# Kernel tuning notes

Measured on AMD Instinct MI355X. Metric: run time of the kernel, lower is better.

The kernel has to match this reference:

```python
import jax, jax.numpy as jnp
import numpy as np

LOC_SCOPE = 3.0
LOC_BIN_SIZE = 0.5
NUM_HEAD_BIN = 12
PER_LOC_BIN = int(LOC_SCOPE / LOC_BIN_SIZE) * 2  # 12
REG_C = PER_LOC_BIN * 4 + 1 + NUM_HEAD_BIN * 2 + 3  # 76


def decode_bbox_target(roi, reg, anchor):
    # roi: (M, 3) point centers; reg: (M, 76); anchor: (3,)
    b = PER_LOC_BIN
    f32 = reg.dtype
    x_bin = jnp.argmax(reg[:, 0:b], axis=1)
    z_bin = jnp.argmax(reg[:, b:2 * b], axis=1)
    pos_x = x_bin.astype(f32) * LOC_BIN_SIZE + LOC_BIN_SIZE / 2 - LOC_SCOPE
    pos_z = z_bin.astype(f32) * LOC_BIN_SIZE + LOC_BIN_SIZE / 2 - LOC_SCOPE
    # fine xz residual: gather residual of the argmax bin (batch_dims=1 gather)
    x_res = jnp.take_along_axis(reg[:, 2 * b:3 * b], x_bin[:, None], axis=1)[:, 0] * LOC_BIN_SIZE
    z_res = jnp.take_along_axis(reg[:, 3 * b:4 * b], z_bin[:, None], axis=1)[:, 0] * LOC_BIN_SIZE
    pos_x = pos_x + x_res
    pos_z = pos_z + z_res
    start = 4 * b
    # y by direct offset (get_y_by_bin=False)
    pos_y = roi[:, 1] + reg[:, start]
    start = start + 1
    # heading: coarse bin argmax + fine residual gather (get_ry_fine=False)
    ry_bin = jnp.argmax(reg[:, start:start + NUM_HEAD_BIN], axis=1)
    ry_res_norm = jnp.take_along_axis(
        reg[:, start + NUM_HEAD_BIN:start + 2 * NUM_HEAD_BIN], ry_bin[:, None], axis=1)[:, 0]
    angle_per_class = 2.0 * np.pi / NUM_HEAD_BIN
    ry = (ry_bin.astype(f32) * angle_per_class + ry_res_norm * (angle_per_class / 2)) % (2.0 * np.pi)
    ry = jnp.where(ry > np.pi, ry - 2.0 * np.pi, ry)
    # size: residual around anchor
    hwl = reg[:, start + 2 * NUM_HEAD_BIN:start + 2 * NUM_HEAD_BIN + 3] * anchor + anchor
    # roi has 3 cols -> no rotate_pc_along_y branch; shift x,z by roi center
    box = jnp.concatenate([
        (pos_x + roi[:, 0])[:, None],
        pos_y[:, None],
        (pos_z + roi[:, 2])[:, None],
        hwl,
        ry[:, None],
    ], axis=1)  # (M, 7)
    return box


def setup_inputs() -> dict:
    key = jax.random.key(0)
    k1, k2, k3 = jax.random.split(key, 3)
    B, N = 8, 131072
    rpn_scores = jax.random.normal(k1, (B, N), dtype=jnp.float32)
    rpn_reg = jax.random.normal(k2, (B, N, REG_C), dtype=jnp.float32)
    xyz = jax.random.normal(k3, (B, N, 3), dtype=jnp.float32) * 20.0
    anchor_size = jnp.array([1.52563191462, 1.62856739989, 3.88311640418], dtype=jnp.float32)
    return {"rpn_scores": rpn_scores, "rpn_reg": rpn_reg, "xyz": xyz, "anchor_size": anchor_size}


def reference(rpn_scores, rpn_reg, xyz, anchor_size):
    B, N, C = rpn_reg.shape
    props = decode_bbox_target(xyz.reshape(-1, 3), rpn_reg.reshape(-1, C), anchor_size)
    props = props.reshape(B, N, 7)
    # post_process: lift y to box top-center (y + h/2)
    props = jnp.concatenate([props[..., :1], props[..., 1:2] + props[..., 3:4] / 2, props[..., 2:]], axis=-1)
    # score-descending ordering of proposals (per batch row)
    order = jnp.argsort(-rpn_scores, axis=1)  # (B, N)
    boxes = jnp.take_along_axis(props, order[..., None], axis=1)
    scores = jnp.take_along_axis(rpn_scores, order, axis=1)
    # pack boxes+scores: (B, N, 8)
    return jnp.concatenate([boxes, scores[..., None]], axis=-1)
```

## Files before the change

kernel.cpp:

```cpp
#include <hip/hip_runtime.h>
#include <math.h>

#define N_PER   131072
#define NBATCH  8
#define REGC    76
#define TOTAL   (NBATCH * N_PER)
#define TILE    2048
#define NBLKSEG (N_PER / TILE)
#define BINS    256
#define SCTH    512
#define CHUNKS  (TILE / SCTH)

__device__ __forceinline__ unsigned desc_key(float f) {
    unsigned u = __float_as_uint(f);
    return (u & 0x80000000u) ? u : ~(u | 0x80000000u);
}

__global__ __launch_bounds__(256) void decode_kernel(
    const float* __restrict__ scores, const float* __restrict__ reg,
    const float* __restrict__ xyz, const float* __restrict__ anchor,
    float* __restrict__ boxes8)
{
    int p = blockIdx.x * 256 + threadIdx.x;
    const float* r = reg + (size_t)p * REGC;
    const float4* r4 = (const float4*)r;

    float4 q0 = r4[0],  q1 = r4[1],  q2 = r4[2];
    float4 q3 = r4[3],  q4 = r4[4],  q5 = r4[5];
    float4 s0 = r4[12], s1 = r4[13], s2 = r4[14], s3 = r4[15];
    float4 tt = r4[18];

    float xa[12] = {q0.x,q0.y,q0.z,q0.w, q1.x,q1.y,q1.z,q1.w, q2.x,q2.y,q2.z,q2.w};
    float za[12] = {q3.x,q3.y,q3.z,q3.w, q4.x,q4.y,q4.z,q4.w, q5.x,q5.y,q5.z,q5.w};
    float ra[12] = {s0.y,s0.z,s0.w, s1.x,s1.y,s1.z,s1.w, s2.x,s2.y,s2.z,s2.w, s3.x};

    int xb = 0; float xm = xa[0];
#pragma unroll
    for (int c = 1; c < 12; ++c) { if (xa[c] > xm) { xm = xa[c]; xb = c; } }
    int zb = 0; float zm = za[0];
#pragma unroll
    for (int c = 1; c < 12; ++c) { if (za[c] > zm) { zm = za[c]; zb = c; } }
    int yb = 0; float ym = ra[0];
#pragma unroll
    for (int c = 1; c < 12; ++c) { if (ra[c] > ym) { ym = ra[c]; yb = c; } }

    float x_res  = r[24 + xb];
    float z_res  = r[36 + zb];
    float ry_res = r[61 + yb];

    float rx = xyz[(size_t)p * 3 + 0];
    float ryy = xyz[(size_t)p * 3 + 1];
    float rz = xyz[(size_t)p * 3 + 2];
    float a0 = anchor[0], a1 = anchor[1], a2 = anchor[2];

    const float APC    = (float)(2.0 * M_PI / 12.0);
    const float HAPC   = (float)(M_PI / 12.0);
    const float TWO_PI = (float)(2.0 * M_PI);
    const float PI_F   = (float)M_PI;

    float vry = __fadd_rn(__fmul_rn((float)yb, APC), __fmul_rn(ry_res, HAPC));
    float m = fmodf(vry, TWO_PI);
    if (m < 0.0f) m += TWO_PI;
    if (m > PI_F) m -= TWO_PI;

    float h = tt.y * a0 + a0;
    float w = tt.z * a1 + a1;
    float l = tt.w * a2 + a2;

    float ox = (((float)xb * 0.5f + 0.25f - 3.0f) + x_res * 0.5f) + rx;
    float oz = (((float)zb * 0.5f + 0.25f - 3.0f) + z_res * 0.5f) + rz;
    float oy = (ryy + s0.x) + h * 0.5f;

    float sc = scores[p];

    float4* ob = (float4*)(boxes8 + (size_t)p * 8);
    ob[0] = make_float4(ox, oy, oz, h);
    ob[1] = make_float4(w, l, m, sc);
}

template<int PASS>
__global__ __launch_bounds__(256) void hist_kernel(
    const float* __restrict__ scores, const unsigned* __restrict__ keyIn,
    unsigned short* __restrict__ hist)
{
    __shared__ unsigned h[BINS];
    int tid = threadIdx.x;
    h[tid] = 0;
    __syncthreads();
    int id = blockIdx.x;
    int seg = id & 7, blk = id >> 3;
    size_t base = (size_t)seg * N_PER + (size_t)blk * TILE;
#pragma unroll
    for (int c = 0; c < TILE / 256; ++c) {
        unsigned key;
        if (PASS == 0) key = desc_key(scores[base + c * 256 + tid]);
        else           key = keyIn[base + c * 256 + tid];
        atomicAdd(&h[(key >> (PASS * 8)) & 255u], 1u);
    }
    __syncthreads();
    hist[(size_t)(seg * NBLKSEG + blk) * BINS + tid] = (unsigned short)h[tid];
}

template<int PASS>
__global__ __launch_bounds__(512) void scatter_kernel(
    const float* __restrict__ scores,
    const unsigned* __restrict__ keyIn, const unsigned* __restrict__ payIn,
    unsigned* __restrict__ keyOut, unsigned* __restrict__ payOut,
    const unsigned short* __restrict__ hist)
{
    __shared__ unsigned whist[CHUNKS * 8][BINS];
    __shared__ unsigned skey[TILE];
    __shared__ unsigned spay[TILE];
    __shared__ unsigned offs[BINS];
    __shared__ unsigned lexcl[BINS];
    __shared__ unsigned wsum[4];

    const int tid  = threadIdx.x;
    const int wave = tid >> 6, lane = tid & 63;
    const unsigned long long lmask = (1ull << lane) - 1ull;
    const int id  = blockIdx.x;
    const int seg = id & 7, blk = id >> 3;
    const size_t segbase = (size_t)seg * N_PER;
    const int gbase = blk * TILE;

    unsigned my_pref = 0, my_tot = 0;
    if (tid < BINS) {
        const unsigned short* hp = hist + (size_t)(seg * NBLKSEG) * BINS + tid;
        unsigned pref = 0, tot = 0;
#pragma unroll
        for (int b = 0; b < NBLKSEG; ++b) {
            unsigned c = hp[(size_t)b * BINS];
            tot += c;
            if (b < blk) pref += c;
        }
        my_pref = pref; my_tot = tot;
    } else {
        int z = tid - BINS;
        unsigned* wf = &whist[0][0];
#pragma unroll
        for (int k = 0; k < CHUNKS * 8; ++k) wf[k * BINS + z] = 0;
    }
    __syncthreads();

    unsigned my_base = 0;
    if (tid < BINS) {
        unsigned v = my_tot;
#pragma unroll
        for (int o = 1; o < 64; o <<= 1) {
            unsigned n = __shfl_up(v, o, 64);
            if (lane >= o) v += n;
        }
        if (lane == 63) wsum[wave] = v;
        my_base = v - my_tot;
    }
    __syncthreads();
    if (tid < BINS) {
        unsigned add = 0;
#pragma unroll
        for (int w2 = 0; w2 < 4; ++w2) { if (w2 < wave) add += wsum[w2]; }
        offs[tid] = my_base + add + my_pref;
    }

    unsigned kr[CHUNKS], pr[CHUNKS], dr[CHUNKS], rr[CHUNKS];
#pragma unroll
    for (int c = 0; c < CHUNKS; ++c) {
        int idx = c * SCTH + tid;
        unsigned key, pay;
        if (PASS == 0) {
            key = desc_key(scores[segbase + gbase + idx]);
            pay = (unsigned)(gbase + idx);
        } else {
            key = keyIn[segbase + gbase + idx];
            pay = payIn[segbase + gbase + idx];
        }
        unsigned d = (key >> (PASS * 8)) & 255u;
        unsigned long long peers = ~0ull;
#pragma unroll
        for (int b = 0; b < 8; ++b) {
            unsigned long long vote = __ballot((d >> b) & 1u);
            peers &= ((d >> b) & 1u) ? vote : ~vote;
        }
        unsigned rank = (unsigned)__popcll(peers & lmask);
        if (rank == 0) whist[c * 8 + wave][d] = (unsigned)__popcll(peers);
        kr[c] = key; pr[c] = pay; dr[c] = d; rr[c] = rank;
    }
    __syncthreads();

    unsigned my_ltot = 0, my_lpart = 0;
    if (tid < BINS) {
        unsigned run = 0;
#pragma unroll
        for (int i = 0; i < CHUNKS * 8; ++i) {
            unsigned v = whist[i][tid];
            whist[i][tid] = run;
            run += v;
        }
        my_ltot = run;
        unsigned v = run;
#pragma unroll
        for (int o = 1; o < 64; o <<= 1) {
            unsigned n = __shfl_up(v, o, 64);
            if (lane >= o) v += n;
        }
        if (lane == 63) wsum[wave] = v;
        my_lpart = v - my_ltot;
    }
    __syncthreads();
    if (tid < BINS) {
        unsigned add = 0;
#pragma unroll
        for (int w2 = 0; w2 < 4; ++w2) { if (w2 < wave) add += wsum[w2]; }
        lexcl[tid] = my_lpart + add;
    }
    __syncthreads();

#pragma unroll
    for (int c = 0; c < CHUNKS; ++c) {
        unsigned j = lexcl[dr[c]] + whist[c * 8 + wave][dr[c]] + rr[c];
        skey[j] = kr[c];
        spay[j] = pr[c];
    }
    __syncthreads();

#pragma unroll
    for (int c = 0; c < CHUNKS; ++c) {
        unsigned j = (unsigned)(c * SCTH + tid);
        unsigned key = skey[j];
        unsigned pay = spay[j];
        unsigned d = (key >> (PASS * 8)) & 255u;
        unsigned g = offs[d] + (j - lexcl[d]);
        if (PASS < 3) keyOut[segbase + g] = key;
        payOut[segbase + g] = pay;
    }
}

__global__ __launch_bounds__(256) void gather_kernel(
    const float* __restrict__ boxes8, const unsigned* __restrict__ pay,
    float* __restrict__ out)
{
    int id = blockIdx.x;
    int seg = id & 7;
    int bi  = id >> 3;
    int t   = threadIdx.x;
    int rowInSeg = bi * 128 + (t >> 1);
    int half = t & 1;
    size_t row = (size_t)seg * N_PER + rowInSeg;
    unsigned i = pay[row];
    const float4* src = (const float4*)(boxes8 + ((size_t)seg * N_PER + i) * 8);
    float4 v = src[half];
    ((float4*)(out + row * 8))[half] = v;
}

extern "C" void kernel_launch(void* const* d_in, const int* in_sizes, int n_in,
                              void* d_out, int out_size, void* d_ws, size_t ws_size,
                              hipStream_t stream)
{
    const float* scores = (const float*)d_in[0];
    const float* reg    = (const float*)d_in[1];
    const float* xyz    = (const float*)d_in[2];
    const float* anchor = (const float*)d_in[3];
    float* out = (float*)d_out;

    char* ws = (char*)d_ws;
    float*    boxes8 = (float*)ws;
    size_t    off    = (size_t)TOTAL * 8 * sizeof(float);
    unsigned* keyA = (unsigned*)(ws + off); off += (size_t)TOTAL * 4;
    unsigned* payA = (unsigned*)(ws + off); off += (size_t)TOTAL * 4;
    unsigned* keyB = (unsigned*)(ws + off); off += (size_t)TOTAL * 4;
    unsigned* payB = (unsigned*)(ws + off); off += (size_t)TOTAL * 4;
    unsigned short* hist = (unsigned short*)(ws + off);
    off += (size_t)NBATCH * NBLKSEG * BINS * sizeof(unsigned short);
    (void)ws_size; (void)in_sizes; (void)n_in; (void)out_size;

    decode_kernel<<<TOTAL / 256, 256, 0, stream>>>(scores, reg, xyz, anchor, boxes8);

    const int NG = NBATCH * NBLKSEG;

    hist_kernel<0><<<NG, 256, 0, stream>>>(scores, nullptr, hist);
    scatter_kernel<0><<<NG, SCTH, 0, stream>>>(scores, nullptr, nullptr,
                                               keyB, payB, hist);
    hist_kernel<1><<<NG, 256, 0, stream>>>(nullptr, keyB, hist);
    scatter_kernel<1><<<NG, SCTH, 0, stream>>>(nullptr, keyB, payB,
                                               keyA, payA, hist);
    hist_kernel<2><<<NG, 256, 0, stream>>>(nullptr, keyA, hist);
    scatter_kernel<2><<<NG, SCTH, 0, stream>>>(nullptr, keyA, payA,
                                               keyB, payB, hist);
    hist_kernel<3><<<NG, 256, 0, stream>>>(nullptr, keyB, hist);
    scatter_kernel<3><<<NG, SCTH, 0, stream>>>(nullptr, keyB, payB,
                                               nullptr, payA, hist);

    gather_kernel<<<NBATCH * (N_PER / 128), 256, 0, stream>>>(boxes8, payA, out);
}
```

Measured before the change: 523.3 us.

## Fuse radix histograms into one pass, add decoupled lookback, spread decode across passes

Computes all four digit histograms in a single kernel, replacing the four per-pass histogram launches. A decoupled-lookback chain across blocks computes each block's per-bin prefix within a scatter pass. The decode work is split into quarters: one quarter runs in the histogram kernel and the rest in scatter passes 0-2. The final gather is folded into the last scatter pass. Keys are also narrowed to 16 and 8 bits in later passes to cut traffic. The aim is fewer launches and less memory traffic, at the cost of spin-wait lookback that relies on blocks being scheduled in a forward-progress order.

```diff
diff --git a/kernel.cpp b/kernel.cpp
--- a/kernel.cpp
+++ b/kernel.cpp
@@ -10,18 +10,28 @@
 #define BINS    256
 #define SCTH    512
 #define CHUNKS  (TILE / SCTH)
+#define NG      (NBATCH * NBLKSEG)
+#define QROWS   (TOTAL / 4)
 
 __device__ __forceinline__ unsigned desc_key(float f) {
     unsigned u = __float_as_uint(f);
     return (u & 0x80000000u) ? u : ~(u | 0x80000000u);
 }
 
-__global__ __launch_bounds__(256) void decode_kernel(
-    const float* __restrict__ scores, const float* __restrict__ reg,
-    const float* __restrict__ xyz, const float* __restrict__ anchor,
+__device__ __forceinline__ unsigned wave_incl_scan(unsigned v, int lane) {
+#pragma unroll
+    for (int o = 1; o < 64; o <<= 1) {
+        unsigned n = __shfl_up(v, o, 64);
+        if (lane >= o) v += n;
+    }
+    return v;
+}
+
+__device__ __forceinline__ void decode_one(
+    int p, const float* __restrict__ scores, const float* __restrict__ reg,
+    const float* __restrict__ xyz, float a0, float a1, float a2,
     float* __restrict__ boxes8)
 {
-    int p = blockIdx.x * 256 + threadIdx.x;
     const float* r = reg + (size_t)p * REGC;
     const float4* r4 = (const float4*)r;
 
@@ -48,10 +58,9 @@
     float z_res  = r[36 + zb];
     float ry_res = r[61 + yb];
 
-    float rx = xyz[(size_t)p * 3 + 0];
+    float rx  = xyz[(size_t)p * 3 + 0];
     float ryy = xyz[(size_t)p * 3 + 1];
-    float rz = xyz[(size_t)p * 3 + 2];
-    float a0 = anchor[0], a1 = anchor[1], a2 = anchor[2];
+    float rz  = xyz[(size_t)p * 3 + 2];
 
     const float APC    = (float)(2.0 * M_PI / 12.0);
     const float HAPC   = (float)(M_PI / 12.0);
@@ -78,39 +87,51 @@
     ob[1] = make_float4(w, l, m, sc);
 }
 
-template<int PASS>
-__global__ __launch_bounds__(256) void hist_kernel(
-    const float* __restrict__ scores, const unsigned* __restrict__ keyIn,
-    unsigned short* __restrict__ hist)
+__global__ __launch_bounds__(256) void hist_decode_kernel(
+    const float* __restrict__ scores, const float* __restrict__ reg,
+    const float* __restrict__ xyz, const float* __restrict__ anchor,
+    float* __restrict__ boxes8, unsigned* __restrict__ ghist)
 {
-    __shared__ unsigned h[BINS];
+    __shared__ unsigned lh[4][BINS];
     int tid = threadIdx.x;
-    h[tid] = 0;
+    lh[0][tid] = 0; lh[1][tid] = 0; lh[2][tid] = 0; lh[3][tid] = 0;
     __syncthreads();
     int id = blockIdx.x;
     int seg = id & 7, blk = id >> 3;
     size_t base = (size_t)seg * N_PER + (size_t)blk * TILE;
 #pragma unroll
     for (int c = 0; c < TILE / 256; ++c) {
-        unsigned key;
-        if (PASS == 0) key = desc_key(scores[base + c * 256 + tid]);
-        else           key = keyIn[base + c * 256 + tid];
-        atomicAdd(&h[(key >> (PASS * 8)) & 255u], 1u);
-    }
-    __syncthreads();
-    hist[(size_t)(seg * NBLKSEG + blk) * BINS + tid] = (unsigned short)h[tid];
+        unsigned k = desc_key(scores[base + c * 256 + tid]);
+        atomicAdd(&lh[0][k & 255u], 1u);
+        atomicAdd(&lh[1][(k >> 8) & 255u], 1u);
+        atomicAdd(&lh[2][(k >> 16) & 255u], 1u);
+        atomicAdd(&lh[3][k >> 24], 1u);
+    }
+    __syncthreads();
+#pragma unroll
+    for (int p = 0; p < 4; ++p)
+        atomicAdd(&ghist[(size_t)(seg * 4 + p) * BINS + tid], lh[p][tid]);
+
+    float a0 = anchor[0], a1 = anchor[1], a2 = anchor[2];
+    int r0 = id * 512 + tid;
+    decode_one(r0,       scores, reg, xyz, a0, a1, a2, boxes8);
+    decode_one(r0 + 256, scores, reg, xyz, a0, a1, a2, boxes8);
 }
 
 template<int PASS>
-__global__ __launch_bounds__(512) void scatter_kernel(
+__global__ __launch_bounds__(SCTH) void scatter_kernel(
     const float* __restrict__ scores,
-    const unsigned* __restrict__ keyIn, const unsigned* __restrict__ payIn,
-    unsigned* __restrict__ keyOut, unsigned* __restrict__ payOut,
-    const unsigned short* __restrict__ hist)
+    const void* __restrict__ keyIn, const unsigned* __restrict__ payIn,
+    void* __restrict__ keyOut, unsigned* __restrict__ payOut,
+    const unsigned* __restrict__ ghist, unsigned* __restrict__ status,
+    const float* __restrict__ reg, const float* __restrict__ xyz,
+    const float* __restrict__ anchor, float* __restrict__ boxes8,
+    float* __restrict__ out)
 {
     __shared__ unsigned whist[CHUNKS * 8][BINS];
-    __shared__ unsigned skey[TILE];
+    __shared__ unsigned skey[(PASS < 3) ? TILE : 1];
     __shared__ unsigned spay[TILE];
+    __shared__ unsigned char sdig[TILE];
     __shared__ unsigned offs[BINS];
     __shared__ unsigned lexcl[BINS];
     __shared__ unsigned wsum[4];
@@ -123,17 +144,12 @@
     const size_t segbase = (size_t)seg * N_PER;
     const int gbase = blk * TILE;
 
-    unsigned my_pref = 0, my_tot = 0;
+    unsigned my_part = 0;
     if (tid < BINS) {
-        const unsigned short* hp = hist + (size_t)(seg * NBLKSEG) * BINS + tid;
-        unsigned pref = 0, tot = 0;
-#pragma unroll
-        for (int b = 0; b < NBLKSEG; ++b) {
-            unsigned c = hp[(size_t)b * BINS];
-            tot += c;
-            if (b < blk) pref += c;
-        }
-        my_pref = pref; my_tot = tot;
+        unsigned tot = ghist[(size_t)(seg * 4 + PASS) * BINS + tid];
+        unsigned v = wave_incl_scan(tot, lane);
+        if (lane == 63) wsum[wave] = v;
+        my_part = v - tot;
     } else {
         int z = tid - BINS;
         unsigned* wf = &whist[0][0];
@@ -141,39 +157,34 @@
         for (int k = 0; k < CHUNKS * 8; ++k) wf[k * BINS + z] = 0;
     }
     __syncthreads();
-
-    unsigned my_base = 0;
-    if (tid < BINS) {
-        unsigned v = my_tot;
-#pragma unroll
-        for (int o = 1; o < 64; o <<= 1) {
-            unsigned n = __shfl_up(v, o, 64);
-            if (lane >= o) v += n;
-        }
-        if (lane == 63) wsum[wave] = v;
-        my_base = v - my_tot;
-    }
-    __syncthreads();
     if (tid < BINS) {
         unsigned add = 0;
 #pragma unroll
         for (int w2 = 0; w2 < 4; ++w2) { if (w2 < wave) add += wsum[w2]; }
-        offs[tid] = my_base + add + my_pref;
+        offs[tid] = my_part + add;
     }
 
     unsigned kr[CHUNKS], pr[CHUNKS], dr[CHUNKS], rr[CHUNKS];
 #pragma unroll
     for (int c = 0; c < CHUNKS; ++c) {
         int idx = c * SCTH + tid;
-        unsigned key, pay;
+        unsigned outkey = 0, d, pay;
         if (PASS == 0) {
-            key = desc_key(scores[segbase + gbase + idx]);
+            unsigned k = desc_key(scores[segbase + gbase + idx]);
+            outkey = k; d = k & 255u;
             pay = (unsigned)(gbase + idx);
+        } else if (PASS == 1) {
+            unsigned k = ((const unsigned*)keyIn)[segbase + gbase + idx];
+            outkey = k >> 16; d = (k >> 8) & 255u;
+            pay = payIn[segbase + gbase + idx];
+        } else if (PASS == 2) {
+            unsigned k = ((const unsigned short*)keyIn)[segbase + gbase + idx];
+            outkey = k >> 8; d = k & 255u;
+            pay = payIn[segbase + gbase + idx];
         } else {
-            key = keyIn[segbase + gbase + idx];
+            d = ((const unsigned char*)keyIn)[segbase + gbase + idx];
             pay = payIn[segbase + gbase + idx];
         }
-        unsigned d = (key >> (PASS * 8)) & 255u;
         unsigned long long peers = ~0ull;
 #pragma unroll
         for (int b = 0; b < 8; ++b) {
@@ -182,11 +193,11 @@
         }
         unsigned rank = (unsigned)__popcll(peers & lmask);
         if (rank == 0) whist[c * 8 + wave][d] = (unsigned)__popcll(peers);
-        kr[c] = key; pr[c] = pay; dr[c] = d; rr[c] = rank;
-    }
-    __syncthreads();
-
-    unsigned my_ltot = 0, my_lpart = 0;
+        kr[c] = outkey; pr[c] = pay; dr[c] = d; rr[c] = rank;
+    }
+    __syncthreads();
+
+    unsigned my_lrun = 0, my_lpart = 0;
     if (tid < BINS) {
         unsigned run = 0;
 #pragma unroll
@@ -195,15 +206,36 @@
             whist[i][tid] = run;
             run += v;
         }
-        my_ltot = run;
-        unsigned v = run;
-#pragma unroll
-        for (int o = 1; o < 64; o <<= 1) {
-            unsigned n = __shfl_up(v, o, 64);
-            if (lane >= o) v += n;
-        }
-        if (lane == 63) wsum[wave] = v;
-        my_lpart = v - my_ltot;
+        my_lrun = run;
+        unsigned* stp = status + (size_t)(seg * NBLKSEG) * BINS + tid;
+        unsigned pref = 0;
+        if (blk == 0) {
+            __hip_atomic_store(&stp[(size_t)blk * BINS],
+                (2u << 20) | ((unsigned)PASS << 18) | run,
+                __ATOMIC_RELEASE, __HIP_MEMORY_SCOPE_AGENT);
+        } else {
+            __hip_atomic_store(&stp[(size_t)blk * BINS],
+                (1u << 20) | ((unsigned)PASS << 18) | run,
+                __ATOMIC_RELEASE, __HIP_MEMORY_SCOPE_AGENT);
+            int b = blk - 1;
+            for (;;) {
+                unsigned v;
+                do {
+                    v = __hip_atomic_load(&stp[(size_t)b * BINS],
+                        __ATOMIC_ACQUIRE, __HIP_MEMORY_SCOPE_AGENT);
+                } while (((v >> 18) & 3u) != (unsigned)PASS || (v >> 20) == 0u);
+                pref += v & 0x3FFFFu;
+                if ((v >> 20) == 2u) break;
+                --b;
+            }
+            __hip_atomic_store(&stp[(size_t)blk * BINS],
+                (2u << 20) | ((unsigned)PASS << 18) | (pref + run),
+                __ATOMIC_RELEASE, __HIP_MEMORY_SCOPE_AGENT);
+        }
+        offs[tid] += pref;
+        unsigned v2 = wave_incl_scan(run, lane);
+        if (lane == 63) wsum[wave] = v2;
+        my_lpart = v2 - run;
     }
     __syncthreads();
     if (tid < BINS) {
@@ -217,38 +249,40 @@
 #pragma unroll
     for (int c = 0; c < CHUNKS; ++c) {
         unsigned j = lexcl[dr[c]] + whist[c * 8 + wave][dr[c]] + rr[c];
-        skey[j] = kr[c];
+        if (PASS < 3) skey[j] = kr[c];
         spay[j] = pr[c];
+        sdig[j] = (unsigned char)dr[c];
     }
     __syncthreads();
 
 #pragma unroll
     for (int c = 0; c < CHUNKS; ++c) {
         unsigned j = (unsigned)(c * SCTH + tid);
-        unsigned key = skey[j];
+        unsigned d = sdig[j];
+        unsigned g = offs[d] + (j - lexcl[d]);
         unsigned pay = spay[j];
-        unsigned d = (key >> (PASS * 8)) & 255u;
-        unsigned g = offs[d] + (j - lexcl[d]);
-        if (PASS < 3) keyOut[segbase + g] = key;
-        payOut[segbase + g] = pay;
-    }
-}
-
-__global__ __launch_bounds__(256) void gather_kernel(
-    const float* __restrict__ boxes8, const unsigned* __restrict__ pay,
-    float* __restrict__ out)
-{
-    int id = blockIdx.x;
-    int seg = id & 7;
-    int bi  = id >> 3;
-    int t   = threadIdx.x;
-    int rowInSeg = bi * 128 + (t >> 1);
-    int half = t & 1;
-    size_t row = (size_t)seg * N_PER + rowInSeg;
-    unsigned i = pay[row];
-    const float4* src = (const float4*)(boxes8 + ((size_t)seg * N_PER + i) * 8);
-    float4 v = src[half];
-    ((float4*)(out + row * 8))[half] = v;
+        if (PASS == 0) {
+            ((unsigned*)keyOut)[segbase + g] = skey[j];
+            payOut[segbase + g] = pay;
+        } else if (PASS == 1) {
+            ((unsigned short*)keyOut)[segbase + g] = (unsigned short)skey[j];
+            payOut[segbase + g] = pay;
+        } else if (PASS == 2) {
+            ((unsigned char*)keyOut)[segbase + g] = (unsigned char)skey[j];
+            payOut[segbase + g] = pay;
+        } else {
+            const float4* src = (const float4*)(boxes8 + (segbase + pay) * 8);
+            float4 v0 = src[0], v1 = src[1];
+            float4* dst = (float4*)(out + (segbase + g) * 8);
+            dst[0] = v0; dst[1] = v1;
+        }
+    }
+
+    if constexpr (PASS < 3) {
+        float a0 = anchor[0], a1 = anchor[1], a2 = anchor[2];
+        int r = (PASS + 1) * QROWS + id * SCTH + tid;
+        decode_one(r, scores, reg, xyz, a0, a1, a2, boxes8);
+    }
 }
 
 extern "C" void kernel_launch(void* const* d_in, const int* in_sizes, int n_in,
@@ -262,32 +296,32 @@
     float* out = (float*)d_out;
 
     char* ws = (char*)d_ws;
-    float*    boxes8 = (float*)ws;
-    size_t    off    = (size_t)TOTAL * 8 * sizeof(float);
-    unsigned* keyA = (unsigned*)(ws + off); off += (size_t)TOTAL * 4;
-    unsigned* payA = (unsigned*)(ws + off); off += (size_t)TOTAL * 4;
-    unsigned* keyB = (unsigned*)(ws + off); off += (size_t)TOTAL * 4;
-    unsigned* payB = (unsigned*)(ws + off); off += (size_t)TOTAL * 4;
-    unsigned short* hist = (unsigned short*)(ws + off);
-    off += (size_t)NBATCH * NBLKSEG * BINS * sizeof(unsigned short);
+    float*          boxes8 = (float*)ws;
+    size_t off = (size_t)TOTAL * 8 * sizeof(float);
+    unsigned*       keyB   = (unsigned*)(ws + off);       off += (size_t)TOTAL * 4;
+    unsigned*       payB   = (unsigned*)(ws + off);       off += (size_t)TOTAL * 4;
+    unsigned short* keyA16 = (unsigned short*)(ws + off); off += (size_t)TOTAL * 2;
+    unsigned*       payA   = (unsigned*)(ws + off);       off += (size_t)TOTAL * 4;
+    unsigned char*  keyC8  = (unsigned char*)(ws + off);  off += (size_t)TOTAL * 1;
+    unsigned*       ghist  = (unsigned*)(ws + off);
+    size_t ghist_bytes  = (size_t)NBATCH * 4 * BINS * 4;
+    off += ghist_bytes;
+    unsigned*       status = (unsigned*)(ws + off);
+    size_t status_bytes = (size_t)NBATCH * NBLKSEG * BINS * 4;
+    off += status_bytes;
     (void)ws_size; (void)in_sizes; (void)n_in; (void)out_size;
 
-    decode_kernel<<<TOTAL / 256, 256, 0, stream>>>(scores, reg, xyz, anchor, boxes8);
-
-    const int NG = NBATCH * NBLKSEG;
-
-    hist_kernel<0><<<NG, 256, 0, stream>>>(scores, nullptr, hist);
+    hipMemsetAsync(ghist, 0, ghist_bytes + status_bytes, stream);
+
+    hist_decode_kernel<<<NG, 256, 0, stream>>>(scores, reg, xyz, anchor,
+                                               boxes8, ghist);
+
     scatter_kernel<0><<<NG, SCTH, 0, stream>>>(scores, nullptr, nullptr,
-                                               keyB, payB, hist);
-    hist_kernel<1><<<NG, 256, 0, stream>>>(nullptr, keyB, hist);
-    scatter_kernel<1><<<NG, SCTH, 0, stream>>>(nullptr, keyB, payB,
-                                               keyA, payA, hist);
-    hist_kernel<2><<<NG, 256, 0, stream>>>(nullptr, keyA, hist);
-    scatter_kernel<2><<<NG, SCTH, 0, stream>>>(nullptr, keyA, payA,
-                                               keyB, payB, hist);
-    hist_kernel<3><<<NG, 256, 0, stream>>>(nullptr, keyB, hist);
-    scatter_kernel<3><<<NG, SCTH, 0, stream>>>(nullptr, keyB, payB,
-                                               nullptr, payA, hist);
-
-    gather_kernel<<<NBATCH * (N_PER / 128), 256, 0, stream>>>(boxes8, payA, out);
-}
+        keyB, payB, ghist, status, reg, xyz, anchor, boxes8, nullptr);
+    scatter_kernel<1><<<NG, SCTH, 0, stream>>>(scores, keyB, payB,
+        keyA16, payA, ghist, status, reg, xyz, anchor, boxes8, nullptr);
+    scatter_kernel<2><<<NG, SCTH, 0, stream>>>(scores, keyA16, payA,
+        keyC8, payB, ghist, status, reg, xyz, anchor, boxes8, nullptr);
+    scatter_kernel<3><<<NG, SCTH, 0, stream>>>(nullptr, keyC8, payB,
+        nullptr, nullptr, ghist, status, nullptr, nullptr, nullptr, boxes8, out);
+}
```

New measurement: 1.412 ms. +169.9%, slower.
